# Kernel tuning notes

Measured on AMD Instinct MI355X. Metric: run time of the kernel, lower is better.

## Reference

```python
import jax, jax.numpy as jnp
import numpy as np


def setup_inputs() -> dict:
    key = jax.random.key(0)
    kx, kw = jax.random.split(key)
    B, IN, OUT = 8192, 1024, 4096
    x = jax.random.normal(kx, (B, IN), dtype=jnp.float32)
    # torch.rand -> uniform [0,1)
    weight = jax.random.uniform(kw, (IN, OUT), dtype=jnp.float32)
    return {"x": x, "weight": weight}


def reference(x, weight):
    # Faithful to: (x.unsqueeze(-1) - weight).pow(2).sum(-2)
    # i.e. out[b, o] = sum_i (x[b, i] - weight[i, o])**2
    # Computed via the squared-distance expansion to avoid the
    # (B, in, out) broadcast intermediate:
    x_sq = jnp.sum(x * x, axis=-1, keepdims=True)          # (B, 1)
    w_sq = jnp.sum(weight * weight, axis=0)                # (OUT,)
    cross = jnp.matmul(x, weight)                          # (B, OUT)
    return x_sq - 2.0 * cross + w_sq
```

## Files before the change

### kernel.cpp

```cpp
#include <hip/hip_runtime.h>
#include <cstdint>
#include <cstddef>

#define B_DIM   8192
#define IN_DIM  1024
#define OUT_DIM 4096

typedef __attribute__((ext_vector_type(8)))  short s16x8;
typedef __attribute__((ext_vector_type(16))) float f32x16;

__device__ __forceinline__ unsigned short f32_to_bf16(float f) {
    unsigned int u = __float_as_uint(f);
    u += 0x7FFFu + ((u >> 16) & 1u);
    return (unsigned short)(u >> 16);
}

__device__ __forceinline__ void async_copy16(const void* gptr, void* ldsptr) {
    __builtin_amdgcn_global_load_lds(
        (__attribute__((address_space(1))) void*)gptr,
        (__attribute__((address_space(3))) void*)ldsptr,
        16, 0, 0);
}

__global__ __launch_bounds__(256) void convert_x_kernel(
    const float* __restrict__ x, unsigned short* __restrict__ xb,
    float* __restrict__ xsq, float* __restrict__ wsq)
{
    const int t  = threadIdx.x;
    const int wv = t >> 6;
    const int l  = t & 63;
    const int b  = blockIdx.x * 4 + wv;

    const float4* src = (const float4*)(x  + (size_t)b * IN_DIM);
    ushort4*      dst = (ushort4*)     (xb + (size_t)b * IN_DIM);

    float s = 0.0f;
    #pragma unroll
    for (int j = 0; j < 4; ++j) {
        float4 v = src[l + 64 * j];
        ushort4 h;
        h.x = f32_to_bf16(v.x);
        h.y = f32_to_bf16(v.y);
        h.z = f32_to_bf16(v.z);
        h.w = f32_to_bf16(v.w);
        dst[l + 64 * j] = h;
        s += v.x * v.x + v.y * v.y + v.z * v.z + v.w * v.w;
    }
    #pragma unroll
    for (int off = 32; off > 0; off >>= 1) s += __shfl_down(s, off, 64);
    if (l == 0) xsq[b] = s;

    if (blockIdx.x < OUT_DIM / 256) wsq[blockIdx.x * 256 + t] = 0.0f;
}

__global__ __launch_bounds__(256) void convert_w_kernel(
    const float* __restrict__ w, unsigned short* __restrict__ wT,
    float* __restrict__ wsq)
{
    __shared__ float tile[64][65];
    const int t  = threadIdx.x;
    const int o0 = blockIdx.x * 64;
    const int i0 = blockIdx.y * 64;

    const int oc = (t & 15) * 4;
    const int ir = t >> 4;
    #pragma unroll
    for (int r = 0; r < 4; ++r) {
        const int i = ir + r * 16;
        float4 v = *(const float4*)(w + (size_t)(i0 + i) * OUT_DIM + o0 + oc);
        tile[i][oc + 0] = v.x;
        tile[i][oc + 1] = v.y;
        tile[i][oc + 2] = v.z;
        tile[i][oc + 3] = v.w;
    }
    __syncthreads();

    const int ol = t >> 2;
    const int c  = t & 3;
    float s = 0.0f;
    s16x8 p0, p1;
    #pragma unroll
    for (int j = 0; j < 8; ++j) {
        float f0 = tile[c * 16 + j][ol];
        float f1 = tile[c * 16 + 8 + j][ol];
        s += f0 * f0 + f1 * f1;
        p0[j] = (short)f32_to_bf16(f0);
        p1[j] = (short)f32_to_bf16(f1);
    }
    s16x8* dstp = (s16x8*)(wT + (size_t)(o0 + ol) * IN_DIM + i0 + c * 16);
    dstp[0] = p0;
    dstp[1] = p1;

    s += __shfl_xor(s, 1, 64);
    s += __shfl_xor(s, 2, 64);
    if (c == 0) atomicAdd(&wsq[o0 + ol], s);
}

__global__ __launch_bounds__(256) void rbf_gemm_kernel(
    const unsigned short* __restrict__ A,
    const unsigned short* __restrict__ Bt,
    const float* __restrict__ xsq,
    const float* __restrict__ wsq,
    float* __restrict__ out)
{
    __shared__ __align__(16) unsigned short As[128 * 64];
    __shared__ __align__(16) unsigned short Bs[128 * 64];

    const int t    = threadIdx.x;
    const int w    = t >> 6;
    const int l    = t & 63;
    const int l32  = l & 31;
    const int half = l >> 5;
    const int tile_m  = blockIdx.x * 128;
    const int tile_n  = blockIdx.y * 128;
    const int waveRow = w >> 1;
    const int waveCol = w & 1;

    f32x16 acc[2][2];
    #pragma unroll
    for (int mi = 0; mi < 2; ++mi)
        #pragma unroll
        for (int ni = 0; ni < 2; ++ni)
            #pragma unroll
            for (int r = 0; r < 16; ++r)
                acc[mi][ni][r] = 0.0f;

    for (int kt = 0; kt < IN_DIM / 64; ++kt) {
        const int k0 = kt * 64;
        #pragma unroll
        for (int it = 0; it < 4; ++it) {
            const int s   = it * 256 + t;
            const int row = s >> 3;
            const int kb  = (s & 7) ^ (row & 7);
            const int ldsbase = (it * 256 + w * 64) * 8;
            async_copy16(A  + (size_t)(tile_m + row) * IN_DIM + k0 + kb * 8,
                         As + ldsbase);
            async_copy16(Bt + (size_t)(tile_n + row) * IN_DIM + k0 + kb * 8,
                         Bs + ldsbase);
        }
        __syncthreads();

        #pragma unroll
        for (int ks = 0; ks < 4; ++ks) {
            const int kb = ks * 2 + half;
            s16x8 af[2], bfr[2];
            #pragma unroll
            for (int mi = 0; mi < 2; ++mi) {
                const int row = waveRow * 64 + mi * 32 + l32;
                af[mi] = *(const s16x8*)(As + row * 64 + (kb ^ (row & 7)) * 8);
            }
            #pragma unroll
            for (int ni = 0; ni < 2; ++ni) {
                const int row = waveCol * 64 + ni * 32 + l32;
                bfr[ni] = *(const s16x8*)(Bs + row * 64 + (kb ^ (row & 7)) * 8);
            }
            #pragma unroll
            for (int mi = 0; mi < 2; ++mi)
                #pragma unroll
                for (int ni = 0; ni < 2; ++ni)
                    acc[mi][ni] = __builtin_amdgcn_mfma_f32_32x32x16_bf16(
                        af[mi], bfr[ni], acc[mi][ni], 0, 0, 0);
        }
        __syncthreads();
    }

    #pragma unroll
    for (int mi = 0; mi < 2; ++mi) {
        const int mbase = tile_m + waveRow * 64 + mi * 32 + 4 * half;
        #pragma unroll
        for (int r2 = 0; r2 < 4; ++r2) {
            #pragma unroll
            for (int r1 = 0; r1 < 4; ++r1) {
                const int m = mbase + r1 + 8 * r2;
                const float xs = xsq[m];
                #pragma unroll
                for (int ni = 0; ni < 2; ++ni) {
                    const int n = tile_n + waveCol * 64 + ni * 32 + l32;
                    out[(size_t)m * OUT_DIM + n] =
                        xs + wsq[n] - 2.0f * acc[mi][ni][r2 * 4 + r1];
                }
            }
        }
    }
}

extern "C" void kernel_launch(void* const* d_in, const int* in_sizes, int n_in,
                              void* d_out, int out_size, void* d_ws, size_t ws_size,
                              hipStream_t stream)
{
    const float* x   = (const float*)d_in[0];
    const float* wgt = (const float*)d_in[1];
    float* out = (float*)d_out;
    char*  ws  = (char*)d_ws;

    unsigned short* xb = (unsigned short*)ws;
    unsigned short* wT = (unsigned short*)(ws + (size_t)B_DIM * IN_DIM * 2);
    float* xsq = (float*)(ws + (size_t)B_DIM * IN_DIM * 2 + (size_t)OUT_DIM * IN_DIM * 2);
    float* wsq = xsq + B_DIM;

    convert_x_kernel<<<B_DIM / 4, 256, 0, stream>>>(x, xb, xsq, wsq);
    convert_w_kernel<<<dim3(OUT_DIM / 64, IN_DIM / 64), 256, 0, stream>>>(wgt, wT, wsq);
    rbf_gemm_kernel<<<dim3(B_DIM / 128, OUT_DIM / 128), 256, 0, stream>>>(xb, wT, xsq, wsq, out);
}
```

Measured before the change: 233.6 us.

## Pre-tile bf16 operands into MFMA fragment layout and drop wsq atomics

The conversion kernels now write x and W as bf16 in a blocked layout of 32x16 fragments, ordered the way the MFMA reads them. Each GEMM async copy and each LDS fragment read then becomes one contiguous 16-byte-per-lane access with no XOR swizzle. The W conversion kernel now loops over all of K per 32-column strip and reduces wsq in shared memory, which removes the zero-initialisation and the atomicAdd. The cost is different access patterns in the conversion kernels and fewer blocks for the W pass (128 blocks), which may underuse the GPU.

After: 242.8 us. 4.0% more time.

```diff
diff --git a/kernel.cpp b/kernel.cpp
--- a/kernel.cpp
+++ b/kernel.cpp
@@ -5,6 +5,7 @@
 #define B_DIM   8192
 #define IN_DIM  1024
 #define OUT_DIM 4096
+#define KT      (IN_DIM / 16)
 
 typedef __attribute__((ext_vector_type(8)))  short s16x8;
 typedef __attribute__((ext_vector_type(16))) float f32x16;
@@ -22,97 +23,103 @@
         16, 0, 0);
 }
 
-__global__ __launch_bounds__(256) void convert_x_kernel(
-    const float* __restrict__ x, unsigned short* __restrict__ xb,
-    float* __restrict__ xsq, float* __restrict__ wsq)
+
+__global__ __launch_bounds__(256) void tile_x_kernel(
+    const float* __restrict__ x, unsigned short* __restrict__ At,
+    float* __restrict__ xsq)
 {
     const int t  = threadIdx.x;
-    const int wv = t >> 6;
+    const int w  = t >> 6;
     const int l  = t & 63;
-    const int b  = blockIdx.x * 4 + wv;
-
-    const float4* src = (const float4*)(x  + (size_t)b * IN_DIM);
-    ushort4*      dst = (ushort4*)     (xb + (size_t)b * IN_DIM);
+    const int mt = blockIdx.x;
+    const int m  = mt * 32 + (l & 31);
+    const int h  = l >> 5;
 
     float s = 0.0f;
     #pragma unroll
-    for (int j = 0; j < 4; ++j) {
-        float4 v = src[l + 64 * j];
-        ushort4 h;
-        h.x = f32_to_bf16(v.x);
-        h.y = f32_to_bf16(v.y);
-        h.z = f32_to_bf16(v.z);
-        h.w = f32_to_bf16(v.w);
-        dst[l + 64 * j] = h;
-        s += v.x * v.x + v.y * v.y + v.z * v.z + v.w * v.w;
-    }
-    #pragma unroll
-    for (int off = 32; off > 0; off >>= 1) s += __shfl_down(s, off, 64);
-    if (l == 0) xsq[b] = s;
-
-    if (blockIdx.x < OUT_DIM / 256) wsq[blockIdx.x * 256 + t] = 0.0f;
-}
-
-__global__ __launch_bounds__(256) void convert_w_kernel(
-    const float* __restrict__ w, unsigned short* __restrict__ wT,
+    for (int c = 0; c < 16; ++c) {
+        const int kt = c * 4 + w;
+        const float* src = x + (size_t)m * IN_DIM + kt * 16 + h * 8;
+        float4 v0 = ((const float4*)src)[0];
+        float4 v1 = ((const float4*)src)[1];
+        s16x8 p;
+        p[0] = (short)f32_to_bf16(v0.x); p[1] = (short)f32_to_bf16(v0.y);
+        p[2] = (short)f32_to_bf16(v0.z); p[3] = (short)f32_to_bf16(v0.w);
+        p[4] = (short)f32_to_bf16(v1.x); p[5] = (short)f32_to_bf16(v1.y);
+        p[6] = (short)f32_to_bf16(v1.z); p[7] = (short)f32_to_bf16(v1.w);
+        *(s16x8*)(At + ((size_t)mt * KT + kt) * 512 + l * 8) = p;
+        s += v0.x*v0.x + v0.y*v0.y + v0.z*v0.z + v0.w*v0.w
+           + v1.x*v1.x + v1.y*v1.y + v1.z*v1.z + v1.w*v1.w;
+    }
+    s += __shfl_down(s, 32, 64);
+    __shared__ float red[4][32];
+    if (l < 32) red[w][l] = s;
+    __syncthreads();
+    if (t < 32) xsq[mt * 32 + t] = red[0][t] + red[1][t] + red[2][t] + red[3][t];
+}
+
+__global__ __launch_bounds__(256) void tile_w_kernel(
+    const float* __restrict__ wgt, unsigned short* __restrict__ Bt,
     float* __restrict__ wsq)
 {
-    __shared__ float tile[64][65];
+    __shared__ float tile[64 * 33];
     const int t  = threadIdx.x;
-    const int o0 = blockIdx.x * 64;
-    const int i0 = blockIdx.y * 64;
-
-    const int oc = (t & 15) * 4;
-    const int ir = t >> 4;
-    #pragma unroll
-    for (int r = 0; r < 4; ++r) {
-        const int i = ir + r * 16;
-        float4 v = *(const float4*)(w + (size_t)(i0 + i) * OUT_DIM + o0 + oc);
-        tile[i][oc + 0] = v.x;
-        tile[i][oc + 1] = v.y;
-        tile[i][oc + 2] = v.z;
-        tile[i][oc + 3] = v.w;
-    }
+    const int w  = t >> 6;
+    const int l  = t & 63;
+    const int nt = blockIdx.x;
+    const int n0 = nt * 32;
+    const int rr = t >> 3;
+    const int cc = t & 7;
+
+    float s = 0.0f;
+    for (int c = 0; c < 16; ++c) {
+        const int k0 = c * 64;
+        __syncthreads();
+        #pragma unroll
+        for (int rep = 0; rep < 2; ++rep) {
+            const int r = rr + rep * 32;
+            float4 v = *(const float4*)(wgt + (size_t)(k0 + r) * OUT_DIM + n0 + cc * 4);
+            float* d = &tile[r * 33 + cc * 4];
+            d[0] = v.x; d[1] = v.y; d[2] = v.z; d[3] = v.w;
+        }
+        __syncthreads();
+        const int kt = c * 4 + w;
+        const int n  = l & 31;
+        const int kb = w * 16 + (l >> 5) * 8;
+        s16x8 p;
+        #pragma unroll
+        for (int j = 0; j < 8; ++j) {
+            float f = tile[(kb + j) * 33 + n];
+            s += f * f;
+            p[j] = (short)f32_to_bf16(f);
+        }
+        *(s16x8*)(Bt + ((size_t)nt * KT + kt) * 512 + l * 8) = p;
+    }
+    s += __shfl_down(s, 32, 64);
+    __shared__ float red[4][32];
+    if (l < 32) red[w][l] = s;
     __syncthreads();
-
-    const int ol = t >> 2;
-    const int c  = t & 3;
-    float s = 0.0f;
-    s16x8 p0, p1;
-    #pragma unroll
-    for (int j = 0; j < 8; ++j) {
-        float f0 = tile[c * 16 + j][ol];
-        float f1 = tile[c * 16 + 8 + j][ol];
-        s += f0 * f0 + f1 * f1;
-        p0[j] = (short)f32_to_bf16(f0);
-        p1[j] = (short)f32_to_bf16(f1);
-    }
-    s16x8* dstp = (s16x8*)(wT + (size_t)(o0 + ol) * IN_DIM + i0 + c * 16);
-    dstp[0] = p0;
-    dstp[1] = p1;
-
-    s += __shfl_xor(s, 1, 64);
-    s += __shfl_xor(s, 2, 64);
-    if (c == 0) atomicAdd(&wsq[o0 + ol], s);
+    if (t < 32) wsq[n0 + t] = red[0][t] + red[1][t] + red[2][t] + red[3][t];
 }
 
 __global__ __launch_bounds__(256) void rbf_gemm_kernel(
-    const unsigned short* __restrict__ A,
+    const unsigned short* __restrict__ At,
     const unsigned short* __restrict__ Bt,
     const float* __restrict__ xsq,
     const float* __restrict__ wsq,
     float* __restrict__ out)
 {
-    __shared__ __align__(16) unsigned short As[128 * 64];
-    __shared__ __align__(16) unsigned short Bs[128 * 64];
+    __shared__ __align__(16) unsigned short sm[32 * 512];
+    unsigned short* As = sm;
+    unsigned short* Bs = sm + 16 * 512;
 
     const int t    = threadIdx.x;
     const int w    = t >> 6;
     const int l    = t & 63;
     const int l32  = l & 31;
     const int half = l >> 5;
-    const int tile_m  = blockIdx.x * 128;
-    const int tile_n  = blockIdx.y * 128;
+    const int bm = blockIdx.x;
+    const int bn = blockIdx.y;
     const int waveRow = w >> 1;
     const int waveCol = w & 1;
 
@@ -125,57 +132,47 @@
             for (int r = 0; r < 16; ++r)
                 acc[mi][ni][r] = 0.0f;
 
-    for (int kt = 0; kt < IN_DIM / 64; ++kt) {
-        const int k0 = kt * 64;
+    for (int kti = 0; kti < 16; ++kti) {
         #pragma unroll
         for (int it = 0; it < 4; ++it) {
-            const int s   = it * 256 + t;
-            const int row = s >> 3;
-            const int kb  = (s & 7) ^ (row & 7);
-            const int ldsbase = (it * 256 + w * 64) * 8;
-            async_copy16(A  + (size_t)(tile_m + row) * IN_DIM + k0 + kb * 8,
-                         As + ldsbase);
-            async_copy16(Bt + (size_t)(tile_n + row) * IN_DIM + k0 + kb * 8,
-                         Bs + ldsbase);
+            async_copy16(At + ((size_t)(bm * 4 + it) * KT + kti * 4 + w) * 512 + l * 8,
+                         As + (it * 4 + w) * 512);
+            async_copy16(Bt + ((size_t)(bn * 4 + it) * KT + kti * 4 + w) * 512 + l * 8,
+                         Bs + (it * 4 + w) * 512);
         }
         __syncthreads();
 
         #pragma unroll
         for (int ks = 0; ks < 4; ++ks) {
-            const int kb = ks * 2 + half;
-            s16x8 af[2], bfr[2];
-            #pragma unroll
-            for (int mi = 0; mi < 2; ++mi) {
-                const int row = waveRow * 64 + mi * 32 + l32;
-                af[mi] = *(const s16x8*)(As + row * 64 + (kb ^ (row & 7)) * 8);
-            }
-            #pragma unroll
-            for (int ni = 0; ni < 2; ++ni) {
-                const int row = waveCol * 64 + ni * 32 + l32;
-                bfr[ni] = *(const s16x8*)(Bs + row * 64 + (kb ^ (row & 7)) * 8);
-            }
+            s16x8 af[2], bf[2];
+            #pragma unroll
+            for (int mi = 0; mi < 2; ++mi)
+                af[mi] = *(const s16x8*)(As + ((waveRow * 2 + mi) * 4 + ks) * 512 + l * 8);
+            #pragma unroll
+            for (int ni = 0; ni < 2; ++ni)
+                bf[ni] = *(const s16x8*)(Bs + ((waveCol * 2 + ni) * 4 + ks) * 512 + l * 8);
             #pragma unroll
             for (int mi = 0; mi < 2; ++mi)
                 #pragma unroll
                 for (int ni = 0; ni < 2; ++ni)
                     acc[mi][ni] = __builtin_amdgcn_mfma_f32_32x32x16_bf16(
-                        af[mi], bfr[ni], acc[mi][ni], 0, 0, 0);
+                        af[mi], bf[ni], acc[mi][ni], 0, 0, 0);
         }
         __syncthreads();
     }
 
     #pragma unroll
     for (int mi = 0; mi < 2; ++mi) {
-        const int mbase = tile_m + waveRow * 64 + mi * 32 + 4 * half;
+        const int mbase = bm * 128 + waveRow * 64 + mi * 32 + 4 * half;
         #pragma unroll
         for (int r2 = 0; r2 < 4; ++r2) {
             #pragma unroll
             for (int r1 = 0; r1 < 4; ++r1) {
-                const int m = mbase + r1 + 8 * r2;
+                const int m  = mbase + r1 + 8 * r2;
                 const float xs = xsq[m];
                 #pragma unroll
                 for (int ni = 0; ni < 2; ++ni) {
-                    const int n = tile_n + waveCol * 64 + ni * 32 + l32;
+                    const int n = bn * 128 + waveCol * 64 + ni * 32 + l32;
                     out[(size_t)m * OUT_DIM + n] =
                         xs + wsq[n] - 2.0f * acc[mi][ni][r2 * 4 + r1];
                 }
@@ -193,12 +190,12 @@
     float* out = (float*)d_out;
     char*  ws  = (char*)d_ws;
 
-    unsigned short* xb = (unsigned short*)ws;
-    unsigned short* wT = (unsigned short*)(ws + (size_t)B_DIM * IN_DIM * 2);
+    unsigned short* At = (unsigned short*)ws;
+    unsigned short* Bt = (unsigned short*)(ws + (size_t)B_DIM * IN_DIM * 2);
     float* xsq = (float*)(ws + (size_t)B_DIM * IN_DIM * 2 + (size_t)OUT_DIM * IN_DIM * 2);
     float* wsq = xsq + B_DIM;
 
-    convert_x_kernel<<<B_DIM / 4, 256, 0, stream>>>(x, xb, xsq, wsq);
-    convert_w_kernel<<<dim3(OUT_DIM / 64, IN_DIM / 64), 256, 0, stream>>>(wgt, wT, wsq);
-    rbf_gemm_kernel<<<dim3(B_DIM / 128, OUT_DIM / 128), 256, 0, stream>>>(xb, wT, xsq, wsq, out);
-}
+    tile_x_kernel<<<B_DIM / 32, 256, 0, stream>>>(x, At, xsq);
+    tile_w_kernel<<<OUT_DIM / 32, 256, 0, stream>>>(wgt, Bt, wsq);
+    rbf_gemm_kernel<<<dim3(B_DIM / 128, OUT_DIM / 128), 256, 0, stream>>>(At, Bt, xsq, wsq, out);
+}
```
